# Performance work log

Hardware: AMD Instinct MI355X
Metric: run time of the kernel (lower is better)

The kernel has to match this reference:

```python
import jax, jax.numpy as jnp
import numpy as np

NUM_ITEM = 2000
DIM_KEY = 256
DIM_VALUE = 128  # number of memory slots
B, T = 256, 512


def setup_inputs() -> dict:
    key = jax.random.key(0)
    ks = jax.random.split(key, 16)
    s = 0.05
    return {
        'item_seq': jax.random.randint(ks[0], (B, T), 0, NUM_ITEM),
        'correct_seq': jax.random.randint(ks[1], (B, T), 0, 2),
        'k_emb': jax.random.normal(ks[2], (NUM_ITEM, DIM_KEY)) * s,
        'v_emb': jax.random.normal(ks[3], (2 * NUM_ITEM, DIM_KEY)) * s,
        'Mk': jax.random.normal(ks[4], (DIM_VALUE, DIM_KEY)) * s,
        'Mv0': jax.random.normal(ks[5], (DIM_VALUE, DIM_KEY)) * s,
        'e_W': jax.random.normal(ks[6], (DIM_KEY, DIM_KEY)) * s,
        'e_b': jnp.zeros((DIM_KEY,)),
        'a_W': jax.random.normal(ks[7], (DIM_KEY, DIM_KEY)) * s,
        'a_b': jnp.zeros((DIM_KEY,)),
        'f_W': jax.random.normal(ks[8], (DIM_KEY, 2 * DIM_KEY)) * s,
        'f_b': jnp.zeros((DIM_KEY,)),
        'p_W': jax.random.normal(ks[9], (1, DIM_KEY)) * s,
        'p_b': jnp.zeros((1,)),
    }


def reference(item_seq, correct_seq, k_emb, v_emb, Mk, Mv0, e_W, e_b, a_W, a_b, f_W, f_b, p_W, p_b):
    num_item = k_emb.shape[0]
    x = item_seq + num_item * correct_seq            # [B, T]
    k = k_emb[item_seq]                              # [B, T, dk]
    v = v_emb[x]                                     # [B, T, dk]
    w = jax.nn.softmax(jnp.einsum('btk,vk->btv', k, Mk), axis=-1)  # [B, T, dv]
    e = jax.nn.sigmoid(v @ e_W.T + e_b)              # erase gate   [B, T, dk]
    a = jnp.tanh(v @ a_W.T + a_b)                    # add vector   [B, T, dk]

    bsz = item_seq.shape[0]
    Mvt0 = jnp.broadcast_to(Mv0[None], (bsz,) + Mv0.shape)  # [B, dv, dk]

    def step(Mvt, inp):
        wt, et, at = inp                              # [B,dv], [B,dk], [B,dk]
        # read uses the memory state BEFORE the update (Mv[:, :-1] in torch)
        read = jnp.einsum('bv,bvk->bk', wt, Mvt)      # [B, dk]
        wt_ = wt[:, :, None]
        Mvt = Mvt * (1.0 - wt_ * et[:, None, :]) + wt_ * at[:, None, :]
        return Mvt, read

    # time-major scan; Mvt stays resident in the carry
    _, reads = jax.lax.scan(
        step, Mvt0,
        (jnp.swapaxes(w, 0, 1), jnp.swapaxes(e, 0, 1), jnp.swapaxes(a, 0, 1)))
    reads = jnp.swapaxes(reads, 0, 1)                 # [B, T, dk]

    f = jnp.tanh(jnp.concatenate([reads, k], axis=-1) @ f_W.T + f_b)  # [B, T, dk]
    # dropout is identity in eval mode
    predict_score = jax.nn.sigmoid(f @ p_W.T + p_b)[..., 0]          # [B, T]
    return predict_score
```

## Files before the change

kernel.cpp:

```cpp
#include <hip/hip_runtime.h>
#include <hip/hip_bf16.h>
#include <hip/hip_fp16.h>


#define T_SEQ 512
#define DK    256
#define DV    128
#define NITEM 2000
#define BT    131072

typedef __attribute__((ext_vector_type(8))) short bf16x8;
typedef __attribute__((ext_vector_type(4))) float f32x4;
typedef _Float16 f16x8 __attribute__((ext_vector_type(8)));

__device__ __forceinline__ float bf2f(unsigned short u) {
    return __uint_as_float(((unsigned int)u) << 16);
}
__device__ __forceinline__ unsigned short f2bf(float x) {
    unsigned int u = __float_as_uint(x);
    return (unsigned short)((u + 0x7fffu + ((u >> 16) & 1u)) >> 16);
}
__device__ __forceinline__ unsigned short f2h(float x) {
    _Float16 h = (_Float16)x;
    return __builtin_bit_cast(unsigned short, h);
}
__device__ __forceinline__ float fast_rcp(float x) { return __builtin_amdgcn_rcpf(x); }
__device__ __forceinline__ float fast_sigmoid(float x) { return fast_rcp(1.f + __expf(-x)); }
__device__ __forceinline__ float fast_tanh(float x) {
    float t = __expf(2.f * x);
    return (t - 1.f) * fast_rcp(t + 1.f);
}
__device__ __forceinline__ f16x8 fma8(f16x8 a, f16x8 b, f16x8 c) {
    return __builtin_elementwise_fma(a, b, c);
}
__device__ __forceinline__ f16x8 splat8(_Float16 x) {
    return (f16x8){x, x, x, x, x, x, x, x};
}
__device__ __forceinline__ _Float16 lo16(unsigned int u) {
    return __builtin_bit_cast(_Float16, (unsigned short)(u & 0xffffu));
}
__device__ __forceinline__ _Float16 hi16(unsigned int u) {
    return __builtin_bit_cast(_Float16, (unsigned short)(u >> 16));
}

__global__ __launch_bounds__(256) void k0_cvt(
    const float* __restrict__ s0, const float* __restrict__ s1,
    const float* __restrict__ s2, const float* __restrict__ s3,
    const float* __restrict__ s4,
    unsigned short* __restrict__ d0, unsigned short* __restrict__ d1,
    unsigned short* __restrict__ d2, unsigned short* __restrict__ d3,
    unsigned short* __restrict__ d4,
    int n0, int n1, int n2, int n3, int n4)
{
    const float* s; unsigned short* d; int n;
    switch (blockIdx.y) {
        case 0:  s = s0; d = d0; n = n0; break;
        case 1:  s = s1; d = d1; n = n1; break;
        case 2:  s = s2; d = d2; n = n2; break;
        case 3:  s = s3; d = d3; n = n3; break;
        default: s = s4; d = d4; n = n4; break;
    }
    int i4 = (blockIdx.x * 256 + threadIdx.x) * 4;
    if (i4 < n) {
        float4 v = *(const float4*)(s + i4);
        ushort4 o;
        o.x = f2bf(v.x); o.y = f2bf(v.y); o.z = f2bf(v.z); o.w = f2bf(v.w);
        *(ushort4*)(d + i4) = o;
    }
}

__global__ __launch_bounds__(256) void k1_wea(
    const int* __restrict__ item_seq, const int* __restrict__ correct_seq,
    const unsigned short* __restrict__ k_bf, const unsigned short* __restrict__ v_bf,
    const unsigned short* __restrict__ Mk_bf,
    const unsigned short* __restrict__ eW_bf, const float* __restrict__ e_b,
    const unsigned short* __restrict__ aW_bf, const float* __restrict__ a_b,
    unsigned short* __restrict__ Wout, unsigned short* __restrict__ EAout)
{
    const int m_tile = blockIdx.x;
    const int n_tile = blockIdx.y;
    const int tid  = threadIdx.x;
    const int lane = tid & 63;
    const int wv   = tid >> 6;

    __shared__ int idx_s[128];
    __shared__ unsigned short A_s[128 * 40];
    __shared__ unsigned short B_s[128 * 40];

    const unsigned short* Atab = (n_tile == 0) ? k_bf : v_bf;
    const unsigned short* Wtab; int wrow0;
    if (n_tile == 0)      { Wtab = Mk_bf; wrow0 = 0;   }
    else if (n_tile == 1) { Wtab = eW_bf; wrow0 = 0;   }
    else if (n_tile == 2) { Wtab = eW_bf; wrow0 = 128; }
    else if (n_tile == 3) { Wtab = aW_bf; wrow0 = 0;   }
    else                  { Wtab = aW_bf; wrow0 = 128; }

    if (tid < 128) {
        int pos = m_tile * 128 + tid;
        int it = item_seq[pos];
        int co = correct_seq[pos];
        idx_s[tid] = (n_tile == 0) ? it : (it + NITEM * co);
    }
    __syncthreads();

    int myrow[4], myc4[4], myidx[4];
    #pragma unroll
    for (int j = 0; j < 4; ++j) {
        int chunk = tid + 256 * j;
        myrow[j] = chunk >> 3;
        myc4[j]  = chunk & 7;
        myidx[j] = idx_s[myrow[j]];
    }

    f32x4 acc[2][8];
    #pragma unroll
    for (int mi = 0; mi < 2; ++mi)
        #pragma unroll
        for (int ni = 0; ni < 8; ++ni)
            acc[mi][ni] = (f32x4){0.f, 0.f, 0.f, 0.f};

    for (int bk = 0; bk < 8; ++bk) {
        int k0 = bk * 32;
        #pragma unroll
        for (int j = 0; j < 4; ++j) {
            int row = myrow[j], c4 = myc4[j];
            *(ushort4*)&A_s[row * 40 + c4 * 4] =
                *(const ushort4*)(Atab + (long)myidx[j] * DK + k0 + c4 * 4);
            *(ushort4*)&B_s[row * 40 + c4 * 4] =
                *(const ushort4*)(Wtab + (long)(wrow0 + row) * DK + k0 + c4 * 4);
        }
        __syncthreads();

        const int kq = lane >> 4;
        const int rr = lane & 15;
        bf16x8 af[2], bfr[8];
        #pragma unroll
        for (int mi = 0; mi < 2; ++mi)
            af[mi] = *(const bf16x8*)&A_s[(wv * 32 + mi * 16 + rr) * 40 + kq * 8];
        #pragma unroll
        for (int ni = 0; ni < 8; ++ni)
            bfr[ni] = *(const bf16x8*)&B_s[(ni * 16 + rr) * 40 + kq * 8];
        #pragma unroll
        for (int ni = 0; ni < 8; ++ni)
            #pragma unroll
            for (int mi = 0; mi < 2; ++mi)
                acc[mi][ni] = __builtin_amdgcn_mfma_f32_16x16x32_bf16(
                    af[mi], bfr[ni], acc[mi][ni], 0, 0, 0);
        __syncthreads();
    }

    const int rowbase = m_tile * 128 + wv * 32;
    const int cgrp = lane >> 4;
    const int cc   = lane & 15;

    if (n_tile == 0) {
        #pragma unroll
        for (int mi = 0; mi < 2; ++mi) {
            #pragma unroll
            for (int i = 0; i < 4; ++i) {
                float m = -1e30f;
                #pragma unroll
                for (int ni = 0; ni < 8; ++ni) m = fmaxf(m, acc[mi][ni][i]);
                m = fmaxf(m, __shfl_xor(m, 1));
                m = fmaxf(m, __shfl_xor(m, 2));
                m = fmaxf(m, __shfl_xor(m, 4));
                m = fmaxf(m, __shfl_xor(m, 8));
                float p[8]; float s = 0.f;
                #pragma unroll
                for (int ni = 0; ni < 8; ++ni) { p[ni] = __expf(acc[mi][ni][i] - m); s += p[ni]; }
                s += __shfl_xor(s, 1); s += __shfl_xor(s, 2);
                s += __shfl_xor(s, 4); s += __shfl_xor(s, 8);
                float inv = fast_rcp(s);
                int row = rowbase + mi * 16 + cgrp * 4 + i;
                #pragma unroll
                for (int ni = 0; ni < 8; ++ni)
                    Wout[(long)row * 128 + ni * 16 + cc] = f2h(p[ni] * inv);
            }
        }
    } else {
        const bool is_e = (n_tile <= 2);
        const float* bias = is_e ? e_b : a_b;
        const int colbase = (is_e ? (n_tile - 1) : (n_tile - 3)) * 128;
        const int sel = is_e ? 0 : 1;
        #pragma unroll
        for (int ni = 0; ni < 8; ++ni) {
            int colp = colbase + ni * 16 + cc;
            float bb = bias[colp];
            #pragma unroll
            for (int mi = 0; mi < 2; ++mi) {
                #pragma unroll
                for (int i = 0; i < 4; ++i) {
                    int row = rowbase + mi * 16 + cgrp * 4 + i;
                    float x = acc[mi][ni][i] + bb;
                    float v = is_e ? -fast_sigmoid(x) : fast_tanh(x);
                    EAout[(long)row * 512 + 2 * colp + sel] = f2h(v);
                }
            }
        }
    }
}

__global__ __launch_bounds__(256, 4) void k2_scan(
    const float* __restrict__ Mv0,
    const unsigned short* __restrict__ Wws,
    const unsigned int* __restrict__ EAws,
    unsigned short* __restrict__ Rws)
{
    const int b    = blockIdx.x >> 1;
    const int kh   = blockIdx.x & 1;
    const int tid  = threadIdx.x;
    const int lane = tid & 63;
    const int wv   = tid >> 6;
    const int row16 = lane & 15;
    const int oct   = lane >> 4;
    const int kw    = kh * 128 + wv * 32;

    f16x8 Mb[4][2];
    #pragma unroll
    for (int vt = 0; vt < 4; ++vt)
        #pragma unroll
        for (int kt = 0; kt < 2; ++kt) {
            f16x8 m;
            #pragma unroll
            for (int j = 0; j < 8; ++j)
                m[j] = (_Float16)Mv0[(vt * 32 + oct * 8 + j) * DK + kw + kt * 16 + row16];
            Mb[vt][kt] = m;
        }

    const long pos0 = (long)b * T_SEQ;

    uint4 wfA[4], wfB[4];
    unsigned int eaA0, eaA1, eaB0, eaB1;
    {
        const unsigned short* wq = Wws + pos0 * 128 + oct * 8;
        wfA[0] = *(const uint4*)(wq);      wfA[1] = *(const uint4*)(wq + 32);
        wfA[2] = *(const uint4*)(wq + 64); wfA[3] = *(const uint4*)(wq + 96);
        wq += 128;
        wfB[0] = *(const uint4*)(wq);      wfB[1] = *(const uint4*)(wq + 32);
        wfB[2] = *(const uint4*)(wq + 64); wfB[3] = *(const uint4*)(wq + 96);
        eaA0 = EAws[pos0 * 256 + kw + row16];
        eaA1 = EAws[pos0 * 256 + kw + 16 + row16];
        eaB0 = EAws[(pos0 + 1) * 256 + kw + row16];
        eaB1 = EAws[(pos0 + 1) * 256 + kw + 16 + row16];
    }

#define K2_STEP(T, WF, EA0, EA1)                                               \
    {                                                                          \
        const uint4 w0 = WF[0], w1 = WF[1], w2 = WF[2], w3 = WF[3];            \
        const unsigned int ea0 = EA0, ea1 = EA1;                               \
        {                                                 \
            long pn = pos0 + ((T) + 2 < T_SEQ ? (T) + 2 : T_SEQ - 1);          \
            const unsigned short* wq = Wws + pn * 128 + oct * 8;               \
            WF[0] = *(const uint4*)(wq);                                       \
            WF[1] = *(const uint4*)(wq + 32);                                  \
            WF[2] = *(const uint4*)(wq + 64);                                  \
            WF[3] = *(const uint4*)(wq + 96);                                  \
            EA0 = EAws[pn * 256 + kw + row16];                                 \
            EA1 = EAws[pn * 256 + kw + 16 + row16];                           \
        }                                                                      \
        const f16x8 w80 = __builtin_bit_cast(f16x8, w0);                       \
        const f16x8 w81 = __builtin_bit_cast(f16x8, w1);                       \
        const f16x8 w82 = __builtin_bit_cast(f16x8, w2);                       \
        const f16x8 w83 = __builtin_bit_cast(f16x8, w3);                       \
          \
        f32x4 D0 = (f32x4){0.f, 0.f, 0.f, 0.f};                                \
        f32x4 D1 = (f32x4){0.f, 0.f, 0.f, 0.f};                                \
        D0 = __builtin_amdgcn_mfma_f32_16x16x32_f16(w80, Mb[0][0], D0, 0,0,0); \
        D0 = __builtin_amdgcn_mfma_f32_16x16x32_f16(w81, Mb[1][0], D0, 0,0,0); \
        D0 = __builtin_amdgcn_mfma_f32_16x16x32_f16(w82, Mb[2][0], D0, 0,0,0); \
        D0 = __builtin_amdgcn_mfma_f32_16x16x32_f16(w83, Mb[3][0], D0, 0,0,0); \
        D1 = __builtin_amdgcn_mfma_f32_16x16x32_f16(w80, Mb[0][1], D1, 0,0,0); \
        D1 = __builtin_amdgcn_mfma_f32_16x16x32_f16(w81, Mb[1][1], D1, 0,0,0); \
        D1 = __builtin_amdgcn_mfma_f32_16x16x32_f16(w82, Mb[2][1], D1, 0,0,0); \
        D1 = __builtin_amdgcn_mfma_f32_16x16x32_f16(w83, Mb[3][1], D1, 0,0,0); \
                       \
        const f16x8 ne80 = splat8(lo16(ea0)), a80 = splat8(hi16(ea0));         \
        const f16x8 ne81 = splat8(lo16(ea1)), a81 = splat8(hi16(ea1));         \
        Mb[0][0] = fma8(w80, fma8(ne80, Mb[0][0], a80), Mb[0][0]);             \
        Mb[1][0] = fma8(w81, fma8(ne80, Mb[1][0], a80), Mb[1][0]);             \
        Mb[2][0] = fma8(w82, fma8(ne80, Mb[2][0], a80), Mb[2][0]);             \
        Mb[3][0] = fma8(w83, fma8(ne80, Mb[3][0], a80), Mb[3][0]);             \
        Mb[0][1] = fma8(w80, fma8(ne81, Mb[0][1], a81), Mb[0][1]);             \
        Mb[1][1] = fma8(w81, fma8(ne81, Mb[1][1], a81), Mb[1][1]);             \
        Mb[2][1] = fma8(w82, fma8(ne81, Mb[2][1], a81), Mb[2][1]);             \
        Mb[3][1] = fma8(w83, fma8(ne81, Mb[3][1], a81), Mb[3][1]);             \
             \
        if (lane < 16) {                                                       \
            unsigned short* rp = Rws + (pos0 + (T)) * 256 + kw + lane;         \
            rp[0]  = f2bf(D0[0]);                                              \
            rp[16] = f2bf(D1[0]);                                              \
        }                                                                      \
    }

    for (int t = 0; t < T_SEQ; t += 2) {
        K2_STEP(t,     wfA, eaA0, eaA1)
        K2_STEP(t + 1, wfB, eaB0, eaB1)
    }
#undef K2_STEP
}

__global__ __launch_bounds__(256) void k3_f(
    const int* __restrict__ item_seq,
    const unsigned short* __restrict__ k_bf,
    const unsigned short* __restrict__ fW_bf, const float* __restrict__ f_b,
    const float* __restrict__ p_W,
    const unsigned short* __restrict__ Rws,
    float* __restrict__ pd)
{
    const int m_tile = blockIdx.x;
    const int nt  = blockIdx.y;
    const int tid = threadIdx.x;
    const int lane = tid & 63;
    const int wv   = tid >> 6;

    __shared__ int idx_s[128];
    __shared__ unsigned short A_s[128 * 40];
    __shared__ unsigned short B_s[128 * 40];

    if (tid < 128) idx_s[tid] = item_seq[m_tile * 128 + tid];
    __syncthreads();

    int myrow[4], myc4[4], myidx[4];
    #pragma unroll
    for (int j = 0; j < 4; ++j) {
        int chunk = tid + 256 * j;
        myrow[j] = chunk >> 3;
        myc4[j]  = chunk & 7;
        myidx[j] = idx_s[myrow[j]];
    }

    f32x4 acc[2][8];
    #pragma unroll
    for (int mi = 0; mi < 2; ++mi)
        #pragma unroll
        for (int ni = 0; ni < 8; ++ni)
            acc[mi][ni] = (f32x4){0.f, 0.f, 0.f, 0.f};

    for (int bk = 0; bk < 16; ++bk) {
        int k0 = bk * 32;
        #pragma unroll
        for (int j = 0; j < 4; ++j) {
            int row = myrow[j], c4 = myc4[j];
            ushort4 ap;
            if (k0 < 256) {
                long pos = (long)m_tile * 128 + row;
                ap = *(const ushort4*)(Rws + pos * 256 + k0 + c4 * 4);
            } else {
                ap = *(const ushort4*)(k_bf + (long)myidx[j] * DK + (k0 - 256) + c4 * 4);
            }
            *(ushort4*)&A_s[row * 40 + c4 * 4] = ap;
            *(ushort4*)&B_s[row * 40 + c4 * 4] =
                *(const ushort4*)(fW_bf + (long)(nt * 128 + row) * 512 + k0 + c4 * 4);
        }
        __syncthreads();

        const int kq = lane >> 4;
        const int rr = lane & 15;
        bf16x8 af[2], bfr[8];
        #pragma unroll
        for (int mi = 0; mi < 2; ++mi)
            af[mi] = *(const bf16x8*)&A_s[(wv * 32 + mi * 16 + rr) * 40 + kq * 8];
        #pragma unroll
        for (int ni = 0; ni < 8; ++ni)
            bfr[ni] = *(const bf16x8*)&B_s[(ni * 16 + rr) * 40 + kq * 8];
        #pragma unroll
        for (int ni = 0; ni < 8; ++ni)
            #pragma unroll
            for (int mi = 0; mi < 2; ++mi)
                acc[mi][ni] = __builtin_amdgcn_mfma_f32_16x16x32_bf16(
                    af[mi], bfr[ni], acc[mi][ni], 0, 0, 0);
        __syncthreads();
    }

    const int rowbase = m_tile * 128 + wv * 32;
    const int cgrp = lane >> 4;
    const int cc   = lane & 15;

    float pw[8];
    #pragma unroll
    for (int ni = 0; ni < 8; ++ni) pw[ni] = p_W[nt * 128 + ni * 16 + cc];

    float s[2][4] = {{0.f,0.f,0.f,0.f},{0.f,0.f,0.f,0.f}};
    #pragma unroll
    for (int ni = 0; ni < 8; ++ni) {
        float bb = f_b[nt * 128 + ni * 16 + cc];
        #pragma unroll
        for (int mi = 0; mi < 2; ++mi)
            #pragma unroll
            for (int i = 0; i < 4; ++i)
                s[mi][i] += fast_tanh(acc[mi][ni][i] + bb) * pw[ni];
    }
    #pragma unroll
    for (int mi = 0; mi < 2; ++mi)
        #pragma unroll
        for (int i = 0; i < 4; ++i) {
            float v = s[mi][i];
            v += __shfl_xor(v, 1); v += __shfl_xor(v, 2);
            v += __shfl_xor(v, 4); v += __shfl_xor(v, 8);
            s[mi][i] = v;
        }
    if (cc == 0) {
        #pragma unroll
        for (int mi = 0; mi < 2; ++mi)
            #pragma unroll
            for (int i = 0; i < 4; ++i)
                pd[(long)nt * BT + rowbase + mi * 16 + cgrp * 4 + i] = s[mi][i];
    }
}

__global__ __launch_bounds__(256) void k4_pred(
    const float* __restrict__ pd, const float* __restrict__ p_b,
    float* __restrict__ out)
{
    int i = blockIdx.x * 256 + threadIdx.x;
    out[i] = fast_sigmoid(pd[i] + pd[BT + i] + p_b[0]);
}

extern "C" void kernel_launch(void* const* d_in, const int* in_sizes, int n_in,
                              void* d_out, int out_size, void* d_ws, size_t ws_size,
                              hipStream_t stream)
{
    const int*   item_seq    = (const int*)d_in[0];
    const int*   correct_seq = (const int*)d_in[1];
    const float* k_emb = (const float*)d_in[2];
    const float* v_emb = (const float*)d_in[3];
    const float* Mk    = (const float*)d_in[4];
    const float* Mv0   = (const float*)d_in[5];
    const float* e_W   = (const float*)d_in[6];
    const float* e_b   = (const float*)d_in[7];
    const float* a_W   = (const float*)d_in[8];
    const float* a_b   = (const float*)d_in[9];
    const float* f_W   = (const float*)d_in[10];
    const float* f_b   = (const float*)d_in[11];
    const float* p_W   = (const float*)d_in[12];
    const float* p_b   = (const float*)d_in[13];
    float* out = (float*)d_out;

    char* ws = (char*)d_ws;
    unsigned short* Wws = (unsigned short*)(ws);
    unsigned short* EAo = (unsigned short*)(ws + 33554432ll);
    unsigned int*   EAi = (unsigned int*)(ws + 33554432ll);
    unsigned short* Rws = (unsigned short*)(ws + 167772160ll);
    float*          pd  = (float*)(ws + 33554432ll);

    unsigned short* kA_bf = Rws;
    unsigned short* v_bf  = Rws + 512000;
    unsigned short* Mk_bf = Rws + 1536000;
    unsigned short* eW_bf = Rws + 1568768;
    unsigned short* aW_bf = Rws + 1634304;
    unsigned short* k3_bf = Wws;
    unsigned short* fW_bf = Wws + 512000;

    k0_cvt<<<dim3(1000, 5), dim3(256), 0, stream>>>(
        k_emb, v_emb, Mk, e_W, a_W,
        kA_bf, v_bf, Mk_bf, eW_bf, aW_bf,
        512000, 1024000, 32768, 65536, 65536);

    k1_wea<<<dim3(1024, 5), dim3(256), 0, stream>>>(
        item_seq, correct_seq, kA_bf, v_bf, Mk_bf, eW_bf, e_b, aW_bf, a_b,
        Wws, EAo);

    k2_scan<<<dim3(512), dim3(256), 0, stream>>>(Mv0, Wws, EAi, Rws);

    k0_cvt<<<dim3(500, 2), dim3(256), 0, stream>>>(
        k_emb, f_W, nullptr, nullptr, nullptr,
        k3_bf, fW_bf, nullptr, nullptr, nullptr,
        512000, 131072, 0, 0, 0);

    k3_f<<<dim3(1024, 2), dim3(256), 0, stream>>>(
        item_seq, k3_bf, fW_bf, f_b, p_W, Rws, pd);

    k4_pred<<<dim3(512), dim3(256), 0, stream>>>(pd, p_b, out);
}
```

Before: 460.8 us.

## Split scan memory state across four blocks per batch to double parallelism

The recurrent scan kernel now gives each batch element four blocks, each owning 64 key columns, instead of two blocks of 128. Each wave then keeps one 16-column tile of the memory state and issues four MFMAs per step instead of eight. The grid grows from 512 to 1024 blocks, which shortens each block's serial dependency chain and should fill more CUs on MI355X. In exchange, the per-step w and erase/add loads are duplicated across twice as many blocks, adding redundant memory traffic.

```diff
diff --git a/kernel.cpp b/kernel.cpp
--- a/kernel.cpp
+++ b/kernel.cpp
@@ -206,31 +206,29 @@
     const unsigned int* __restrict__ EAws,
     unsigned short* __restrict__ Rws)
 {
-    const int b    = blockIdx.x >> 1;
-    const int kh   = blockIdx.x & 1;
+    const int b    = blockIdx.x >> 2;
+    const int kqd  = blockIdx.x & 3;
     const int tid  = threadIdx.x;
     const int lane = tid & 63;
     const int wv   = tid >> 6;
     const int row16 = lane & 15;
     const int oct   = lane >> 4;
-    const int kw    = kh * 128 + wv * 32;
-
-    f16x8 Mb[4][2];
-    #pragma unroll
-    for (int vt = 0; vt < 4; ++vt)
-        #pragma unroll
-        for (int kt = 0; kt < 2; ++kt) {
-            f16x8 m;
-            #pragma unroll
-            for (int j = 0; j < 8; ++j)
-                m[j] = (_Float16)Mv0[(vt * 32 + oct * 8 + j) * DK + kw + kt * 16 + row16];
-            Mb[vt][kt] = m;
-        }
+    const int kw    = kqd * 64 + wv * 16;
+
+    f16x8 Mb[4];
+    #pragma unroll
+    for (int vt = 0; vt < 4; ++vt) {
+        f16x8 m;
+        #pragma unroll
+        for (int j = 0; j < 8; ++j)
+            m[j] = (_Float16)Mv0[(vt * 32 + oct * 8 + j) * DK + kw + row16];
+        Mb[vt] = m;
+    }
 
     const long pos0 = (long)b * T_SEQ;
 
     uint4 wfA[4], wfB[4];
-    unsigned int eaA0, eaA1, eaB0, eaB1;
+    unsigned int eaA, eaB;
     {
         const unsigned short* wq = Wws + pos0 * 128 + oct * 8;
         wfA[0] = *(const uint4*)(wq);      wfA[1] = *(const uint4*)(wq + 32);
@@ -238,16 +236,14 @@
         wq += 128;
         wfB[0] = *(const uint4*)(wq);      wfB[1] = *(const uint4*)(wq + 32);
         wfB[2] = *(const uint4*)(wq + 64); wfB[3] = *(const uint4*)(wq + 96);
-        eaA0 = EAws[pos0 * 256 + kw + row16];
-        eaA1 = EAws[pos0 * 256 + kw + 16 + row16];
-        eaB0 = EAws[(pos0 + 1) * 256 + kw + row16];
-        eaB1 = EAws[(pos0 + 1) * 256 + kw + 16 + row16];
-    }
-
-#define K2_STEP(T, WF, EA0, EA1)                                               \
+        eaA = EAws[pos0 * 256 + kw + row16];
+        eaB = EAws[(pos0 + 1) * 256 + kw + row16];
+    }
+
+#define K2_STEP(T, WF, EA)                                                     \
     {                                                                          \
         const uint4 w0 = WF[0], w1 = WF[1], w2 = WF[2], w3 = WF[3];            \
-        const unsigned int ea0 = EA0, ea1 = EA1;                               \
+        const unsigned int ea = EA;                                            \
         {                                                 \
             long pn = pos0 + ((T) + 2 < T_SEQ ? (T) + 2 : T_SEQ - 1);          \
             const unsigned short* wq = Wws + pn * 128 + oct * 8;               \
@@ -255,46 +251,32 @@
             WF[1] = *(const uint4*)(wq + 32);                                  \
             WF[2] = *(const uint4*)(wq + 64);                                  \
             WF[3] = *(const uint4*)(wq + 96);                                  \
-            EA0 = EAws[pn * 256 + kw + row16];                                 \
-            EA1 = EAws[pn * 256 + kw + 16 + row16];                           \
+            EA = EAws[pn * 256 + kw + row16];                                  \
         }                                                                      \
         const f16x8 w80 = __builtin_bit_cast(f16x8, w0);                       \
         const f16x8 w81 = __builtin_bit_cast(f16x8, w1);                       \
         const f16x8 w82 = __builtin_bit_cast(f16x8, w2);                       \
         const f16x8 w83 = __builtin_bit_cast(f16x8, w3);                       \
-          \
-        f32x4 D0 = (f32x4){0.f, 0.f, 0.f, 0.f};                                \
-        f32x4 D1 = (f32x4){0.f, 0.f, 0.f, 0.f};                                \
-        D0 = __builtin_amdgcn_mfma_f32_16x16x32_f16(w80, Mb[0][0], D0, 0,0,0); \
-        D0 = __builtin_amdgcn_mfma_f32_16x16x32_f16(w81, Mb[1][0], D0, 0,0,0); \
-        D0 = __builtin_amdgcn_mfma_f32_16x16x32_f16(w82, Mb[2][0], D0, 0,0,0); \
-        D0 = __builtin_amdgcn_mfma_f32_16x16x32_f16(w83, Mb[3][0], D0, 0,0,0); \
-        D1 = __builtin_amdgcn_mfma_f32_16x16x32_f16(w80, Mb[0][1], D1, 0,0,0); \
-        D1 = __builtin_amdgcn_mfma_f32_16x16x32_f16(w81, Mb[1][1], D1, 0,0,0); \
-        D1 = __builtin_amdgcn_mfma_f32_16x16x32_f16(w82, Mb[2][1], D1, 0,0,0); \
-        D1 = __builtin_amdgcn_mfma_f32_16x16x32_f16(w83, Mb[3][1], D1, 0,0,0); \
+           \
+        f32x4 D = (f32x4){0.f, 0.f, 0.f, 0.f};                                 \
+        D = __builtin_amdgcn_mfma_f32_16x16x32_f16(w80, Mb[0], D, 0, 0, 0);    \
+        D = __builtin_amdgcn_mfma_f32_16x16x32_f16(w81, Mb[1], D, 0, 0, 0);    \
+        D = __builtin_amdgcn_mfma_f32_16x16x32_f16(w82, Mb[2], D, 0, 0, 0);    \
+        D = __builtin_amdgcn_mfma_f32_16x16x32_f16(w83, Mb[3], D, 0, 0, 0);    \
                        \
-        const f16x8 ne80 = splat8(lo16(ea0)), a80 = splat8(hi16(ea0));         \
-        const f16x8 ne81 = splat8(lo16(ea1)), a81 = splat8(hi16(ea1));         \
-        Mb[0][0] = fma8(w80, fma8(ne80, Mb[0][0], a80), Mb[0][0]);             \
-        Mb[1][0] = fma8(w81, fma8(ne80, Mb[1][0], a80), Mb[1][0]);             \
-        Mb[2][0] = fma8(w82, fma8(ne80, Mb[2][0], a80), Mb[2][0]);             \
-        Mb[3][0] = fma8(w83, fma8(ne80, Mb[3][0], a80), Mb[3][0]);             \
-        Mb[0][1] = fma8(w80, fma8(ne81, Mb[0][1], a81), Mb[0][1]);             \
-        Mb[1][1] = fma8(w81, fma8(ne81, Mb[1][1], a81), Mb[1][1]);             \
-        Mb[2][1] = fma8(w82, fma8(ne81, Mb[2][1], a81), Mb[2][1]);             \
-        Mb[3][1] = fma8(w83, fma8(ne81, Mb[3][1], a81), Mb[3][1]);             \
-             \
-        if (lane < 16) {                                                       \
-            unsigned short* rp = Rws + (pos0 + (T)) * 256 + kw + lane;         \
-            rp[0]  = f2bf(D0[0]);                                              \
-            rp[16] = f2bf(D1[0]);                                              \
-        }                                                                      \
+        const f16x8 ne8 = splat8(lo16(ea)), a8 = splat8(hi16(ea));             \
+        Mb[0] = fma8(w80, fma8(ne8, Mb[0], a8), Mb[0]);                        \
+        Mb[1] = fma8(w81, fma8(ne8, Mb[1], a8), Mb[1]);                        \
+        Mb[2] = fma8(w82, fma8(ne8, Mb[2], a8), Mb[2]);                        \
+        Mb[3] = fma8(w83, fma8(ne8, Mb[3], a8), Mb[3]);                        \
+              \
+        if (lane < 16)                                                         \
+            Rws[(pos0 + (T)) * 256 + kw + lane] = f2bf(D[0]);                  \
     }
 
     for (int t = 0; t < T_SEQ; t += 2) {
-        K2_STEP(t,     wfA, eaA0, eaA1)
-        K2_STEP(t + 1, wfB, eaB0, eaB1)
+        K2_STEP(t,     wfA, eaA)
+        K2_STEP(t + 1, wfB, eaB)
     }
 #undef K2_STEP
 }
@@ -460,7 +442,7 @@
         item_seq, correct_seq, kA_bf, v_bf, Mk_bf, eW_bf, e_b, aW_bf, a_b,
         Wws, EAo);
 
-    k2_scan<<<dim3(512), dim3(256), 0, stream>>>(Mv0, Wws, EAi, Rws);
+    k2_scan<<<dim3(1024), dim3(256), 0, stream>>>(Mv0, Wws, EAi, Rws);
 
     k0_cvt<<<dim3(500, 2), dim3(256), 0, stream>>>(
         k_emb, f_W, nullptr, nullptr, nullptr,
```

After: 497.2 us. 1.08x slower.

## Interleave two batch sequences per scan block to hide serial dependency latency

Applied to the files above, without the earlier changes.

The scan kernel now has each block process two batch elements, keeping two independent memory states in registers and alternating steps between them. This gives the scheduler independent MFMA and FMA chains to overlap within a wave, hiding the latency of the serial recurrence. The grid is halved to 256 blocks, so fewer waves run across the device, and register pressure rises (launch bounds relaxed to 1 block per SM), which may reduce occupancy.

```diff
diff --git a/kernel.cpp b/kernel.cpp
--- a/kernel.cpp
+++ b/kernel.cpp
@@ -200,13 +200,13 @@
     }
 }
 
-__global__ __launch_bounds__(256, 4) void k2_scan(
+__global__ __launch_bounds__(256, 1) void k2_scan(
     const float* __restrict__ Mv0,
     const unsigned short* __restrict__ Wws,
     const unsigned int* __restrict__ EAws,
     unsigned short* __restrict__ Rws)
 {
-    const int b    = blockIdx.x >> 1;
+    const int bp   = blockIdx.x >> 1;
     const int kh   = blockIdx.x & 1;
     const int tid  = threadIdx.x;
     const int lane = tid & 63;
@@ -215,7 +215,7 @@
     const int oct   = lane >> 4;
     const int kw    = kh * 128 + wv * 32;
 
-    f16x8 Mb[4][2];
+    f16x8 Mb0[4][2], Mb1[4][2];
     #pragma unroll
     for (int vt = 0; vt < 4; ++vt)
         #pragma unroll
@@ -224,77 +224,92 @@
             #pragma unroll
             for (int j = 0; j < 8; ++j)
                 m[j] = (_Float16)Mv0[(vt * 32 + oct * 8 + j) * DK + kw + kt * 16 + row16];
-            Mb[vt][kt] = m;
-        }
-
-    const long pos0 = (long)b * T_SEQ;
-
-    uint4 wfA[4], wfB[4];
-    unsigned int eaA0, eaA1, eaB0, eaB1;
+            Mb0[vt][kt] = m;
+            Mb1[vt][kt] = m;
+        }
+
+    const long p0 = (long)(bp * 2)     * T_SEQ;
+    const long p1 = (long)(bp * 2 + 1) * T_SEQ;
+
+    uint4 wfA0[4], wfB0[4], wfA1[4], wfB1[4];
+    unsigned int eaA00, eaA01, eaB00, eaB01;
+    unsigned int eaA10, eaA11, eaB10, eaB11;
     {
-        const unsigned short* wq = Wws + pos0 * 128 + oct * 8;
-        wfA[0] = *(const uint4*)(wq);      wfA[1] = *(const uint4*)(wq + 32);
-        wfA[2] = *(const uint4*)(wq + 64); wfA[3] = *(const uint4*)(wq + 96);
+        const unsigned short* wq = Wws + p0 * 128 + oct * 8;
+        wfA0[0] = *(const uint4*)(wq);      wfA0[1] = *(const uint4*)(wq + 32);
+        wfA0[2] = *(const uint4*)(wq + 64); wfA0[3] = *(const uint4*)(wq + 96);
         wq += 128;
-        wfB[0] = *(const uint4*)(wq);      wfB[1] = *(const uint4*)(wq + 32);
-        wfB[2] = *(const uint4*)(wq + 64); wfB[3] = *(const uint4*)(wq + 96);
-        eaA0 = EAws[pos0 * 256 + kw + row16];
-        eaA1 = EAws[pos0 * 256 + kw + 16 + row16];
-        eaB0 = EAws[(pos0 + 1) * 256 + kw + row16];
-        eaB1 = EAws[(pos0 + 1) * 256 + kw + 16 + row16];
-    }
-
-#define K2_STEP(T, WF, EA0, EA1)                                               \
+        wfB0[0] = *(const uint4*)(wq);      wfB0[1] = *(const uint4*)(wq + 32);
+        wfB0[2] = *(const uint4*)(wq + 64); wfB0[3] = *(const uint4*)(wq + 96);
+        wq = Wws + p1 * 128 + oct * 8;
+        wfA1[0] = *(const uint4*)(wq);      wfA1[1] = *(const uint4*)(wq + 32);
+        wfA1[2] = *(const uint4*)(wq + 64); wfA1[3] = *(const uint4*)(wq + 96);
+        wq += 128;
+        wfB1[0] = *(const uint4*)(wq);      wfB1[1] = *(const uint4*)(wq + 32);
+        wfB1[2] = *(const uint4*)(wq + 64); wfB1[3] = *(const uint4*)(wq + 96);
+        eaA00 = EAws[p0 * 256 + kw + row16];
+        eaA01 = EAws[p0 * 256 + kw + 16 + row16];
+        eaB00 = EAws[(p0 + 1) * 256 + kw + row16];
+        eaB01 = EAws[(p0 + 1) * 256 + kw + 16 + row16];
+        eaA10 = EAws[p1 * 256 + kw + row16];
+        eaA11 = EAws[p1 * 256 + kw + 16 + row16];
+        eaB10 = EAws[(p1 + 1) * 256 + kw + row16];
+        eaB11 = EAws[(p1 + 1) * 256 + kw + 16 + row16];
+    }
+
+#define K2_STEP(T, POS0, WF, EA0, EA1, MB)                                     \
     {                                                                          \
         const uint4 w0 = WF[0], w1 = WF[1], w2 = WF[2], w3 = WF[3];            \
         const unsigned int ea0 = EA0, ea1 = EA1;                               \
         {                                                 \
-            long pn = pos0 + ((T) + 2 < T_SEQ ? (T) + 2 : T_SEQ - 1);          \
+            long pn = (POS0) + ((T) + 2 < T_SEQ ? (T) + 2 : T_SEQ - 1);        \
             const unsigned short* wq = Wws + pn * 128 + oct * 8;               \
             WF[0] = *(const uint4*)(wq);                                       \
             WF[1] = *(const uint4*)(wq + 32);                                  \
             WF[2] = *(const uint4*)(wq + 64);                                  \
             WF[3] = *(const uint4*)(wq + 96);                                  \
             EA0 = EAws[pn * 256 + kw + row16];                                 \
-            EA1 = EAws[pn * 256 + kw + 16 + row16];                           \
+            EA1 = EAws[pn * 256 + kw + 16 + row16];                            \
         }                                                                      \
         const f16x8 w80 = __builtin_bit_cast(f16x8, w0);                       \
         const f16x8 w81 = __builtin_bit_cast(f16x8, w1);                       \
         const f16x8 w82 = __builtin_bit_cast(f16x8, w2);                       \
         const f16x8 w83 = __builtin_bit_cast(f16x8, w3);                       \
-          \
+           \
         f32x4 D0 = (f32x4){0.f, 0.f, 0.f, 0.f};                                \
         f32x4 D1 = (f32x4){0.f, 0.f, 0.f, 0.f};                                \
-        D0 = __builtin_amdgcn_mfma_f32_16x16x32_f16(w80, Mb[0][0], D0, 0,0,0); \
-        D0 = __builtin_amdgcn_mfma_f32_16x16x32_f16(w81, Mb[1][0], D0, 0,0,0); \
-        D0 = __builtin_amdgcn_mfma_f32_16x16x32_f16(w82, Mb[2][0], D0, 0,0,0); \
-        D0 = __builtin_amdgcn_mfma_f32_16x16x32_f16(w83, Mb[3][0], D0, 0,0,0); \
-        D1 = __builtin_amdgcn_mfma_f32_16x16x32_f16(w80, Mb[0][1], D1, 0,0,0); \
-        D1 = __builtin_amdgcn_mfma_f32_16x16x32_f16(w81, Mb[1][1], D1, 0,0,0); \
-        D1 = __builtin_amdgcn_mfma_f32_16x16x32_f16(w82, Mb[2][1], D1, 0,0,0); \
-        D1 = __builtin_amdgcn_mfma_f32_16x16x32_f16(w83, Mb[3][1], D1, 0,0,0); \
+        D0 = __builtin_amdgcn_mfma_f32_16x16x32_f16(w80, MB[0][0], D0, 0,0,0); \
+        D0 = __builtin_amdgcn_mfma_f32_16x16x32_f16(w81, MB[1][0], D0, 0,0,0); \
+        D0 = __builtin_amdgcn_mfma_f32_16x16x32_f16(w82, MB[2][0], D0, 0,0,0); \
+        D0 = __builtin_amdgcn_mfma_f32_16x16x32_f16(w83, MB[3][0], D0, 0,0,0); \
+        D1 = __builtin_amdgcn_mfma_f32_16x16x32_f16(w80, MB[0][1], D1, 0,0,0); \
+        D1 = __builtin_amdgcn_mfma_f32_16x16x32_f16(w81, MB[1][1], D1, 0,0,0); \
+        D1 = __builtin_amdgcn_mfma_f32_16x16x32_f16(w82, MB[2][1], D1, 0,0,0); \
+        D1 = __builtin_amdgcn_mfma_f32_16x16x32_f16(w83, MB[3][1], D1, 0,0,0); \
                        \
         const f16x8 ne80 = splat8(lo16(ea0)), a80 = splat8(hi16(ea0));         \
         const f16x8 ne81 = splat8(lo16(ea1)), a81 = splat8(hi16(ea1));         \
-        Mb[0][0] = fma8(w80, fma8(ne80, Mb[0][0], a80), Mb[0][0]);             \
-        Mb[1][0] = fma8(w81, fma8(ne80, Mb[1][0], a80), Mb[1][0]);             \
-        Mb[2][0] = fma8(w82, fma8(ne80, Mb[2][0], a80), Mb[2][0]);             \
-        Mb[3][0] = fma8(w83, fma8(ne80, Mb[3][0], a80), Mb[3][0]);             \
-        Mb[0][1] = fma8(w80, fma8(ne81, Mb[0][1], a81), Mb[0][1]);             \
-        Mb[1][1] = fma8(w81, fma8(ne81, Mb[1][1], a81), Mb[1][1]);             \
-        Mb[2][1] = fma8(w82, fma8(ne81, Mb[2][1], a81), Mb[2][1]);             \
-        Mb[3][1] = fma8(w83, fma8(ne81, Mb[3][1], a81), Mb[3][1]);             \
-             \
+        MB[0][0] = fma8(w80, fma8(ne80, MB[0][0], a80), MB[0][0]);             \
+        MB[1][0] = fma8(w81, fma8(ne80, MB[1][0], a80), MB[1][0]);             \
+        MB[2][0] = fma8(w82, fma8(ne80, MB[2][0], a80), MB[2][0]);             \
+        MB[3][0] = fma8(w83, fma8(ne80, MB[3][0], a80), MB[3][0]);             \
+        MB[0][1] = fma8(w80, fma8(ne81, MB[0][1], a81), MB[0][1]);             \
+        MB[1][1] = fma8(w81, fma8(ne81, MB[1][1], a81), MB[1][1]);             \
+        MB[2][1] = fma8(w82, fma8(ne81, MB[2][1], a81), MB[2][1]);             \
+        MB[3][1] = fma8(w83, fma8(ne81, MB[3][1], a81), MB[3][1]);             \
+              \
         if (lane < 16) {                                                       \
-            unsigned short* rp = Rws + (pos0 + (T)) * 256 + kw + lane;         \
+            unsigned short* rp = Rws + ((POS0) + (T)) * 256 + kw + lane;       \
             rp[0]  = f2bf(D0[0]);                                              \
             rp[16] = f2bf(D1[0]);                                              \
         }                                                                      \
     }
 
     for (int t = 0; t < T_SEQ; t += 2) {
-        K2_STEP(t,     wfA, eaA0, eaA1)
-        K2_STEP(t + 1, wfB, eaB0, eaB1)
+        K2_STEP(t,     p0, wfA0, eaA00, eaA01, Mb0)
+        K2_STEP(t,     p1, wfA1, eaA10, eaA11, Mb1)
+        K2_STEP(t + 1, p0, wfB0, eaB00, eaB01, Mb0)
+        K2_STEP(t + 1, p1, wfB1, eaB10, eaB11, Mb1)
     }
 #undef K2_STEP
 }
@@ -460,7 +475,7 @@
         item_seq, correct_seq, kA_bf, v_bf, Mk_bf, eW_bf, e_b, aW_bf, a_b,
         Wws, EAo);
 
-    k2_scan<<<dim3(512), dim3(256), 0, stream>>>(Mv0, Wws, EAi, Rws);
+    k2_scan<<<dim3(256), dim3(256), 0, stream>>>(Mv0, Wws, EAi, Rws);
 
     k0_cvt<<<dim3(500, 2), dim3(256), 0, stream>>>(
         k_emb, f_W, nullptr, nullptr, nullptr,
```

New measurement: 489.7 us. +6.3%, slower.
